# Kernel tuning notes

Measured on AMD Instinct MI355X. Metric: run time of the kernel, lower is better.

The kernel has to match this reference:

```python
import jax, jax.numpy as jnp
import numpy as np
from jax import lax

EPS = 2.220446049250313e-16  # np.finfo(float).eps, as in the torch source
DN3 = ('NCDHW', 'OIDHW', 'NCDHW')
DN2 = ('NCHW', 'OIHW', 'NCHW')


def setup_inputs() -> dict:
    key = jax.random.key(0)
    k1, k2, k3 = jax.random.split(key, 3)
    x = jax.random.normal(k1, (256, 256), dtype=jnp.float32)
    filts_temp = jax.random.normal(k2, (8, 1, 2, 9, 9), dtype=jnp.float32)    # [Ft,1,T=2,kh,kw]
    filts_notemp = jax.random.normal(k3, (8, 1, 1, 9, 9), dtype=jnp.float32)  # [Fn,1,1,kh,kw]
    return {"x": x, "filts_temp": filts_temp, "filts_notemp": filts_notemp, "num_rfs": 2}


def _forward(x, filts_temp, filts_notemp, num_rfs):
    kh, kw = filts_temp.shape[3], filts_temp.shape[4]
    corr_x = num_rfs * kh  # torch uses shape[3]
    corr_y = num_rfs * kw  # torch uses shape[4]
    num_filts = filts_temp.shape[0] + filts_notemp.shape[0]

    # x -> [1,1,2,H,W]: duplicate the frame along a temporal axis of length 2
    xv = jnp.broadcast_to(x, (2,) + x.shape)[None, None]

    # fixed-filter temporal conv3d + ReLU (halved)
    x_temp = jax.nn.relu(
        lax.conv_general_dilated(xv, filts_temp, (1, 1, 1), 'VALID', dimension_numbers=DN3) / 2
    )  # [1,Ft,1,H',W']
    # non-temporal conv on the last time slice
    x_notemp = jax.nn.relu(
        lax.conv_general_dilated(xv[:, :, -1:, :, :], filts_notemp, (1, 1, 1), 'VALID',
                                 dimension_numbers=DN3)
    )  # [1,Fn,1,H',W']

    xc = jnp.concatenate([x_temp, x_notemp], axis=1)  # [1,nf,1,H',W']
    # normalize across the filter channel (divisive normalization)
    x1 = xc / (jnp.sum(xc, axis=1, keepdims=True) + EPS)

    H_, W_ = x1.shape[3], x1.shape[4]
    x1f = x1[0, :, 0]  # [nf,H',W']
    # central crop used as correlation templates
    templates = x1f[:, corr_y:H_ - corr_y, corr_x:W_ - corr_x]  # [nf, H'-2cy, W'-2cx]

    # windowed pairwise cross-channel correlation: the torch conv3d with depth-kernel 1
    # is exactly a batched 2D valid cross-correlation (batch = depth index j,
    # out-channel = template index i)
    out = lax.conv_general_dilated(x1f[:, None], templates[:, None], (1, 1), 'VALID',
                                   dimension_numbers=DN2)  # [j, i, 2cy+1, 2cx+1]
    x2 = jnp.transpose(out, (1, 0, 2, 3))[None]  # [1, i, j, 2cy+1, 2cx+1]
    # note: source divides by (y_max-2*corr_y)*(x_max-2*corr_y) (corr_y twice) -- kept faithful
    x2 = x2 / ((H_ - 2 * corr_y) * (W_ - 2 * corr_y))

    x1_out = x1f[None, None]  # [1,1,nf,H',W']
    return (x1_out, x2)


def reference(x, filts_temp, filts_notemp, num_rfs):
    return _forward(x, filts_temp, filts_notemp, num_rfs)
```

## Files before the change

kernel.cpp:

```cpp
#include <hip/hip_runtime.h>
#include <cstdint>

typedef unsigned short u16;
typedef unsigned int   u32;
typedef unsigned long long u64;
typedef __bf16 bf16x8 __attribute__((ext_vector_type(8)));
typedef float  f32x16 __attribute__((ext_vector_type(16)));
typedef float  f32x4  __attribute__((ext_vector_type(4)));
typedef u32    u32x4  __attribute__((ext_vector_type(4)));

#define OUT1 984064
#define OUT2 350464

#define XD_STRIDE  2031616
#define TMPL_OFFB  16252928
#define PART_OFFB  17801216
#define PART_ELEMS (6*OUT2)
#define XC_OFFB    26212352

__global__ __launch_bounds__(256) void k1_conv(
    const float* __restrict__ x, const float* __restrict__ ft,
    const float* __restrict__ fnt, float* __restrict__ out1,
    u16* __restrict__ Xc) {
  __shared__ float xt[24][25];
  __shared__ float wsm[1296];
  const int tid = threadIdx.x;
  const int lx = tid & 15, ly = tid >> 4;
  const int bx = blockIdx.x, by = blockIdx.y;
  for (int idx = tid; idx < 1296; idx += 256) {
    int c = idx / 81, s = idx - (idx / 81) * 81;
    wsm[idx] = (c < 8) ? 0.5f * (ft[c*162 + s] + ft[c*162 + 81 + s])
                       : fnt[(c-8)*81 + s];
  }
  for (int idx = tid; idx < 576; idx += 256) {
    int ry = idx / 24, rx = idx - ry * 24;
    int gy = by*16 + ry; gy = gy > 255 ? 255 : gy;
    int gx = bx*16 + rx; gx = gx > 255 ? 255 : gx;
    xt[ry][rx] = x[gy*256 + gx];
  }
  __syncthreads();
  const int xg = bx*16 + lx, yg = by*16 + ly;
  if (yg >= 248) return;
  float s[16];
#pragma unroll
  for (int c = 0; c < 16; ++c) s[c] = 0.f;
  const bool valid = (xg < 248);
  if (valid) {
#pragma unroll
    for (int u = 0; u < 9; ++u)
#pragma unroll
      for (int v = 0; v < 9; ++v) {
        float xv = xt[ly + u][lx + v];
#pragma unroll
        for (int c = 0; c < 16; ++c)
          s[c] = __builtin_fmaf(xv, wsm[c*81 + u*9 + v], s[c]);
      }
    float sum = 2.2204460492503131e-16f;
#pragma unroll
    for (int c = 0; c < 16; ++c) { s[c] = s[c] > 0.f ? s[c] : 0.f; sum += s[c]; }
    float inv = 1.f / sum;
#pragma unroll
    for (int c = 0; c < 16; ++c) s[c] *= inv;
  }
#pragma unroll
  for (int c = 0; c < 16; ++c) {
    u16 hb = 0;
    if (valid) {
      out1[c*61504 + yg*248 + xg] = s[c];
      u32 ub = __builtin_bit_cast(u32, s[c]);
      hb = (u16)((ub + 0x7fffu + ((ub >> 16) & 1u)) >> 16);
    }
    if (xg < 264) Xc[(c*248 + yg)*264 + xg] = hb;
  }
}

__global__ __launch_bounds__(256) void k1b_expand(
    const u16* __restrict__ Xc, u16* __restrict__ ws16, float* __restrict__ partial) {
  const int cid = blockIdx.x*256 + threadIdx.x;
  for (int z = cid; z < PART_ELEMS; z += 4346*256) partial[z] = 0.f;
  const u32* src = (const u32*)Xc;
  if (cid < 1015808) {
    int n  = cid & 15;
    int r1 = cid >> 4;
    int row = r1 % 248;
    int r2  = r1 / 248;
    int vb  = r2 & 31;
    int d   = r2 >> 5;
    int colb = (d & ~1) + 8*vb;
    int so = (n*248 + row)*132 + (colb >> 1);
    u32 a0 = src[so], a1 = src[so+1], a2 = src[so+2], a3 = src[so+3], a4 = src[so+4];
    u32x4 v;
    if (d & 1) {
      v[0] = (a0 >> 16) | (a1 << 16); v[1] = (a1 >> 16) | (a2 << 16);
      v[2] = (a2 >> 16) | (a3 << 16); v[3] = (a3 >> 16) | (a4 << 16);
    } else { v[0] = a0; v[1] = a1; v[2] = a2; v[3] = a3; }
    *(u32x4*)(ws16 + (size_t)cid*8) = v;
  } else if (cid < 1015808 + 96768) {
    int t  = cid - 1015808;
    int o  = t & 15;
    int r1 = t >> 4;
    int tr = r1 % 216;
    int vb = r1 / 216;
    u32x4 v = {0u, 0u, 0u, 0u};
    if (tr < 212 && vb < 27) {
      int so = (o*248 + tr + 18)*132 + ((18 + 8*vb) >> 1);
      v[0] = src[so]; v[1] = src[so+1]; v[2] = src[so+2]; v[3] = src[so+3];
      if (vb == 26) { v[2] = 0u; v[3] = 0u; }
    }
    *(u32x4*)(ws16 + (size_t)(TMPL_OFFB/2) + (size_t)t*8) = v;
  }
}

#define F_LD(k,m,c) fl[(k)*1024 + (((m)&3) + 4*((m)>>3))*64 + ((c) + 32*(((m)>>2)&1))]

#define LOADA(q,SO) asm volatile("buffer_load_dwordx4 %0, %1, %2, %3 offen" \
  : "=v"(A[q]) : "v"(voffA[q]), "s"(srdA), "s"(SO));
#define LOADB(t,SO) asm volatile("buffer_load_dwordx4 %0, %1, %2, %3 offen" \
  : "=v"(B[t]) : "v"(voffB[t]), "s"(srdB), "s"(SO));
#define WT(N,X,Y) asm volatile("s_waitcnt vmcnt(" #N ")" : "+v"(X), "+v"(Y) ::);
#define MF5(t) { bf16x8 _bb = __builtin_bit_cast(bf16x8, B[t]); \
  acc[0]=__builtin_amdgcn_mfma_f32_32x32x16_bf16(__builtin_bit_cast(bf16x8,A[t+0]),_bb,acc[0],0,0,0); \
  acc[1]=__builtin_amdgcn_mfma_f32_32x32x16_bf16(__builtin_bit_cast(bf16x8,A[t+1]),_bb,acc[1],0,0,0); \
  acc[2]=__builtin_amdgcn_mfma_f32_32x32x16_bf16(__builtin_bit_cast(bf16x8,A[t+2]),_bb,acc[2],0,0,0); \
  acc[3]=__builtin_amdgcn_mfma_f32_32x32x16_bf16(__builtin_bit_cast(bf16x8,A[t+3]),_bb,acc[3],0,0,0); \
  acc[4]=__builtin_amdgcn_mfma_f32_32x32x16_bf16(__builtin_bit_cast(bf16x8,A[t+4]),_bb,acc[4],0,0,0); }

__global__ __launch_bounds__(256, 2) void k2_corr(
    const u16* __restrict__ Ximg2, const u16* __restrict__ Tmpl2,
    float* __restrict__ partial) {
  __shared__ float fl[5120];
  const int bid = blockIdx.x;
  const int d   = bid & 7;
  const int m0  = bid >> 3;
  const int jq  = m0 % 5;
  const int cmb = m0 / 5;
  const int g   = cmb & 3;
  const int uq  = cmb >> 2;
  const int j   = d + 8*jq;
  if (j >= 37) return;
  const int U0  = 72*uq;
  const int R0  = 10*g + U0;
  const int tid  = threadIdx.x;
  const int lane = tid & 63;
  const int w    = tid >> 6;
  const int fn16 = lane & 15;
  const int fuu  = (lane >> 4) & 1;
  const int fg   = lane >> 5;

  u64 pa = (u64)((const char*)Ximg2 + d*XD_STRIDE + jq*63488);
  u64 pb = (u64)((const char*)Tmpl2);
  u32x4 srdA = { (u32)pa, (u32)(pa >> 32), 0xFFFFFFFFu, 0x00020000u };
  u32x4 srdB = { (u32)pb, (u32)(pb >> 32), 0xFFFFFFFFu, 0x00020000u };
  int voffA[13], voffB[9];
#pragma unroll
  for (int q = 0; q < 13; ++q) {
    int r = R0 + fuu + 18*w + 2*q;
    if (r > 247) r = 247;
    voffA[q] = fg*63488 + fn16*16 + r*256;
  }
#pragma unroll
  for (int t = 0; t < 9; ++t)
    voffB[t] = fg*55296 + fn16*16 + (U0 + fuu + 18*w + 2*t)*256;

  f32x16 acc[5];
#pragma unroll
  for (int k = 0; k < 5; ++k)
#pragma unroll
    for (int q = 0; q < 16; ++q) acc[k][q] = 0.f;

  u32x4 A[13], B[9];
  { int sa = 0, sb = 0;
    LOADA(0,sa) LOADB(0,sb) LOADA(1,sa) LOADB(1,sb)
    LOADA(2,sa) LOADB(2,sb) LOADA(3,sa) LOADB(3,sb)
    LOADA(4,sa) LOADB(4,sb) LOADA(5,sa) LOADB(5,sb)
    LOADA(6,sa) LOADB(6,sb) LOADA(7,sa) LOADB(7,sb)
    LOADA(8,sa) LOADA(9,sa) LOADA(10,sa) LOADA(11,sa) LOADA(12,sa) LOADB(8,sb) }

#pragma unroll 1
  for (int sv = 0; sv < 13; ++sv) {
    const int sa = (sv + 1)*126976, sb = (sv + 1)*110592;
    WT(13, A[4],  B[0])  MF5(0) LOADA(0,sa) LOADB(0,sb)
    WT(13, A[5],  B[1])  MF5(1) LOADA(1,sa) LOADB(1,sb)
    WT(13, A[6],  B[2])  MF5(2) LOADA(2,sa) LOADB(2,sb)
    WT(13, A[7],  B[3])  MF5(3) LOADA(3,sa) LOADB(3,sb)
    WT(13, A[8],  B[4])  MF5(4) LOADA(4,sa) LOADB(4,sb)
    WT(14, A[9],  B[5])  MF5(5) LOADA(5,sa) LOADB(5,sb)
    WT(15, A[10], B[6])  MF5(6) LOADA(6,sa) LOADB(6,sb)
    WT(16, A[11], B[7])  MF5(7) LOADA(7,sa) LOADB(7,sb)
    WT(16, A[12], B[8])  MF5(8)
    LOADA(8,sa) LOADA(9,sa) LOADA(10,sa) LOADA(11,sa) LOADA(12,sa) LOADB(8,sb)
  }
  WT(13, A[4],  B[0])  MF5(0)
  WT(11, A[5],  B[1])  MF5(1)
  WT(9,  A[6],  B[2])  MF5(2)
  WT(7,  A[7],  B[3])  MF5(3)
  WT(5,  A[8],  B[4])  MF5(4)
  WT(4,  A[9],  B[5])  MF5(5)
  WT(3,  A[10], B[6])  MF5(6)
  WT(2,  A[11], B[7])  MF5(7)
  WT(0,  A[12], B[8])  MF5(8)
  __syncthreads();

  for (int z = tid; z < 5120; z += 256) fl[z] = 0.f;
  __syncthreads();
  for (int ww = 0; ww < 4; ++ww) {
    if (w == ww) {
#pragma unroll
      for (int k = 0; k < 5; ++k) {
        if (!(g == 3 && k == 4)) {
#pragma unroll
          for (int q = 0; q < 16; ++q)
            fl[k*1024 + q*64 + lane] += acc[k][q];
        }
      }
    }
    __syncthreads();
  }

  const int n = (tid >> 4) & 15;
  const int o = tid & 15;
  float* slab = partial + (uq*2 + (g & 1)) * OUT2;
  for (int ii = 0; ii < 11; ++ii) {
    const int i = 10*g - 1 + ii;
    if (i < 0 || i >= 37) continue;
    const int dd = ii - 1;
    float v;
    if (!(dd & 1)) {
      const int k = dd >> 1;
      v = F_LD(k, n, o) + F_LD(k, n+16, o+16);
    } else {
      v = 0.f;
      if (dd >= 1) v += F_LD((dd-1) >> 1, n+16, o);
      const int kr = (dd+1) >> 1;
      if (kr <= 4) v += F_LD(kr, n, o+16);
    }
    slab[(o*16 + n)*1369 + i*37 + j] = v;
  }
}

__global__ __launch_bounds__(256) void k3_reduce(
    const float* __restrict__ partial, float* __restrict__ out2) {
  const int idx = blockIdx.x*256 + threadIdx.x;
  if (idx >= OUT2/4) return;
  f32x4 s = {0.f, 0.f, 0.f, 0.f};
#pragma unroll
  for (int t = 0; t < 6; ++t) {
    f32x4 v = *(const f32x4*)(partial + t*OUT2 + idx*4);
    s[0] += v[0]; s[1] += v[1]; s[2] += v[2]; s[3] += v[3];
  }
  const float sc = 1.0f / 44944.0f;
  s[0] *= sc; s[1] *= sc; s[2] *= sc; s[3] *= sc;
  *(f32x4*)(out2 + idx*4) = s;
}

extern "C" void kernel_launch(void* const* d_in, const int* in_sizes, int n_in,
                              void* d_out, int out_size, void* d_ws, size_t ws_size,
                              hipStream_t stream) {
  (void)in_sizes; (void)n_in; (void)out_size; (void)ws_size;
  const float* x   = (const float*)d_in[0];
  const float* ft  = (const float*)d_in[1];
  const float* fnt = (const float*)d_in[2];
  float* out = (float*)d_out;
  char*  ws  = (char*)d_ws;
  u16*   Ximg2   = (u16*)ws;
  u16*   Tmpl2   = (u16*)(ws + TMPL_OFFB);
  float* partial = (float*)(ws + PART_OFFB);
  u16*   Xc      = (u16*)(ws + XC_OFFB);

  k1_conv<<<dim3(17, 16), 256, 0, stream>>>(x, ft, fnt, out, Xc);
  k1b_expand<<<4346, 256, 0, stream>>>(Xc, (u16*)ws, partial);
  k2_corr<<<480, 256, 0, stream>>>(Ximg2, Tmpl2, partial);
  k3_reduce<<<343, 256, 0, stream>>>(partial, out + OUT1);
}
```

Baseline: 74.54 us.

## Switch correlation GEMM operands from bf16 to fp8 e4m3 with repacked layout

```diff
diff --git a/kernel.cpp b/kernel.cpp
--- a/kernel.cpp
+++ b/kernel.cpp
@@ -1,22 +1,23 @@
 #include <hip/hip_runtime.h>
+#include <hip/hip_fp8.h>
 #include <cstdint>
 
 typedef unsigned short u16;
 typedef unsigned int   u32;
 typedef unsigned long long u64;
-typedef __bf16 bf16x8 __attribute__((ext_vector_type(8)));
 typedef float  f32x16 __attribute__((ext_vector_type(16)));
 typedef float  f32x4  __attribute__((ext_vector_type(4)));
+typedef u32    u32x2  __attribute__((ext_vector_type(2)));
 typedef u32    u32x4  __attribute__((ext_vector_type(4)));
 
 #define OUT1 984064
 #define OUT2 350464
 
-#define XD_STRIDE  2031616
+#define XD5        1015808
 #define TMPL_OFFB  16252928
-#define PART_OFFB  17801216
+#define PART_OFFB  17027072
 #define PART_ELEMS (6*OUT2)
-#define XC_OFFB    26212352
+#define XC_OFFB    25438208
 
 __global__ __launch_bounds__(256) void k1_conv(
     const float* __restrict__ x, const float* __restrict__ ft,
@@ -70,73 +71,103 @@
       u32 ub = __builtin_bit_cast(u32, s[c]);
       hb = (u16)((ub + 0x7fffu + ((ub >> 16) & 1u)) >> 16);
     }
-    if (xg < 264) Xc[(c*248 + yg)*264 + xg] = hb;
-  }
+    Xc[(c*248 + yg)*272 + xg] = hb;
+  }
+}
+
+__device__ __forceinline__ u32 pk4_fp8(u32 b0, u32 b1) {
+  float f0 = __builtin_bit_cast(float, b0 << 16);
+  float f1 = __builtin_bit_cast(float, b0 & 0xFFFF0000u);
+  float f2 = __builtin_bit_cast(float, b1 << 16);
+  float f3 = __builtin_bit_cast(float, b1 & 0xFFFF0000u);
+  __hip_fp8_e4m3 e0(f0), e1(f1), e2(f2), e3(f3);
+  return (u32)e0.__x | ((u32)e1.__x << 8) | ((u32)e2.__x << 16) | ((u32)e3.__x << 24);
 }
 
 __global__ __launch_bounds__(256) void k1b_expand(
-    const u16* __restrict__ Xc, u16* __restrict__ ws16, float* __restrict__ partial) {
+    const u16* __restrict__ Xc, unsigned char* __restrict__ ws8,
+    float* __restrict__ partial) {
   const int cid = blockIdx.x*256 + threadIdx.x;
-  for (int z = cid; z < PART_ELEMS; z += 4346*256) partial[z] = 0.f;
+  for (int z = cid; z < PART_ELEMS; z += gridDim.x*256) partial[z] = 0.f;
   const u32* src = (const u32*)Xc;
   if (cid < 1015808) {
     int n  = cid & 15;
     int r1 = cid >> 4;
     int row = r1 % 248;
     int r2  = r1 / 248;
-    int vb  = r2 & 31;
-    int d   = r2 >> 5;
-    int colb = (d & ~1) + 8*vb;
-    int so = (n*248 + row)*132 + (colb >> 1);
-    u32 a0 = src[so], a1 = src[so+1], a2 = src[so+2], a3 = src[so+3], a4 = src[so+4];
-    u32x4 v;
+    int vp  = r2 & 15;
+    int d   = r2 >> 4;
+    int col0 = d + 16*vp;
+    int so = (n*248 + row)*136 + (col0 >> 1);
+    u32 a[9], b[8];
+#pragma unroll
+    for (int i = 0; i < 9; ++i) a[i] = src[so + i];
     if (d & 1) {
-      v[0] = (a0 >> 16) | (a1 << 16); v[1] = (a1 >> 16) | (a2 << 16);
-      v[2] = (a2 >> 16) | (a3 << 16); v[3] = (a3 >> 16) | (a4 << 16);
-    } else { v[0] = a0; v[1] = a1; v[2] = a2; v[3] = a3; }
-    *(u32x4*)(ws16 + (size_t)cid*8) = v;
-  } else if (cid < 1015808 + 96768) {
+#pragma unroll
+      for (int i = 0; i < 8; ++i) b[i] = (a[i] >> 16) | (a[i+1] << 16);
+    } else {
+#pragma unroll
+      for (int i = 0; i < 8; ++i) b[i] = a[i];
+    }
+    u32x4 v = { pk4_fp8(b[0], b[1]), pk4_fp8(b[2], b[3]),
+                pk4_fp8(b[4], b[5]), pk4_fp8(b[6], b[7]) };
+    *(u32x4*)(ws8 + ((size_t)((d*16 + vp)*248 + row))*256 + n*16) = v;
+  } else if (cid < 1015808 + 48384) {
     int t  = cid - 1015808;
     int o  = t & 15;
     int r1 = t >> 4;
     int tr = r1 % 216;
-    int vb = r1 / 216;
+    int vp = r1 / 216;
     u32x4 v = {0u, 0u, 0u, 0u};
-    if (tr < 212 && vb < 27) {
-      int so = (o*248 + tr + 18)*132 + ((18 + 8*vb) >> 1);
-      v[0] = src[so]; v[1] = src[so+1]; v[2] = src[so+2]; v[3] = src[so+3];
-      if (vb == 26) { v[2] = 0u; v[3] = 0u; }
-    }
-    *(u32x4*)(ws16 + (size_t)(TMPL_OFFB/2) + (size_t)t*8) = v;
+    if (tr < 212) {
+      int so = (o*248 + tr + 18)*136 + ((18 + 16*vp) >> 1);
+      u32 b[8];
+#pragma unroll
+      for (int i = 0; i < 8; ++i) b[i] = src[so + i];
+      v[0] = pk4_fp8(b[0], b[1]);
+      if (vp < 13) {
+        v[1] = pk4_fp8(b[2], b[3]);
+        v[2] = pk4_fp8(b[4], b[5]);
+        v[3] = pk4_fp8(b[6], b[7]);
+      }
+    }
+    *(u32x4*)(ws8 + TMPL_OFFB + ((size_t)(vp*216 + tr))*256 + o*16) = v;
   }
 }
 
 #define F_LD(k,m,c) fl[(k)*1024 + (((m)&3) + 4*((m)>>3))*64 + ((c) + 32*(((m)>>2)&1))]
 
-#define LOADA(q,SO) asm volatile("buffer_load_dwordx4 %0, %1, %2, %3 offen" \
+#define LD_A(q,SO) asm volatile("buffer_load_dwordx4 %0, %1, %2, %3 offen" \
   : "=v"(A[q]) : "v"(voffA[q]), "s"(srdA), "s"(SO));
-#define LOADB(t,SO) asm volatile("buffer_load_dwordx4 %0, %1, %2, %3 offen" \
+#define LD_B(t,SO) asm volatile("buffer_load_dwordx4 %0, %1, %2, %3 offen" \
   : "=v"(B[t]) : "v"(voffB[t]), "s"(srdB), "s"(SO));
 #define WT(N,X,Y) asm volatile("s_waitcnt vmcnt(" #N ")" : "+v"(X), "+v"(Y) ::);
-#define MF5(t) { bf16x8 _bb = __builtin_bit_cast(bf16x8, B[t]); \
-  acc[0]=__builtin_amdgcn_mfma_f32_32x32x16_bf16(__builtin_bit_cast(bf16x8,A[t+0]),_bb,acc[0],0,0,0); \
-  acc[1]=__builtin_amdgcn_mfma_f32_32x32x16_bf16(__builtin_bit_cast(bf16x8,A[t+1]),_bb,acc[1],0,0,0); \
-  acc[2]=__builtin_amdgcn_mfma_f32_32x32x16_bf16(__builtin_bit_cast(bf16x8,A[t+2]),_bb,acc[2],0,0,0); \
-  acc[3]=__builtin_amdgcn_mfma_f32_32x32x16_bf16(__builtin_bit_cast(bf16x8,A[t+3]),_bb,acc[3],0,0,0); \
-  acc[4]=__builtin_amdgcn_mfma_f32_32x32x16_bf16(__builtin_bit_cast(bf16x8,A[t+4]),_bb,acc[4],0,0,0); }
+#define LO8(V) __builtin_bit_cast(long, (u32x2){(V)[0], (V)[1]})
+#define HI8(V) __builtin_bit_cast(long, (u32x2){(V)[2], (V)[3]})
+#define MF10(t) { long _bl = LO8(B[t]), _bh = HI8(B[t]); \
+  acc[0]=__builtin_amdgcn_mfma_f32_32x32x16_fp8_fp8(LO8(A[t+0]),_bl,acc[0],0,0,0); \
+  acc[1]=__builtin_amdgcn_mfma_f32_32x32x16_fp8_fp8(LO8(A[t+1]),_bl,acc[1],0,0,0); \
+  acc[2]=__builtin_amdgcn_mfma_f32_32x32x16_fp8_fp8(LO8(A[t+2]),_bl,acc[2],0,0,0); \
+  acc[3]=__builtin_amdgcn_mfma_f32_32x32x16_fp8_fp8(LO8(A[t+3]),_bl,acc[3],0,0,0); \
+  acc[4]=__builtin_amdgcn_mfma_f32_32x32x16_fp8_fp8(LO8(A[t+4]),_bl,acc[4],0,0,0); \
+  acc[0]=__builtin_amdgcn_mfma_f32_32x32x16_fp8_fp8(HI8(A[t+0]),_bh,acc[0],0,0,0); \
+  acc[1]=__builtin_amdgcn_mfma_f32_32x32x16_fp8_fp8(HI8(A[t+1]),_bh,acc[1],0,0,0); \
+  acc[2]=__builtin_amdgcn_mfma_f32_32x32x16_fp8_fp8(HI8(A[t+2]),_bh,acc[2],0,0,0); \
+  acc[3]=__builtin_amdgcn_mfma_f32_32x32x16_fp8_fp8(HI8(A[t+3]),_bh,acc[3],0,0,0); \
+  acc[4]=__builtin_amdgcn_mfma_f32_32x32x16_fp8_fp8(HI8(A[t+4]),_bh,acc[4],0,0,0); }
 
 __global__ __launch_bounds__(256, 2) void k2_corr(
-    const u16* __restrict__ Ximg2, const u16* __restrict__ Tmpl2,
+    const unsigned char* __restrict__ Ximg5, const unsigned char* __restrict__ Tmpl5,
     float* __restrict__ partial) {
   __shared__ float fl[5120];
   const int bid = blockIdx.x;
-  const int d   = bid & 7;
+  const int jl  = bid & 7;
   const int m0  = bid >> 3;
-  const int jq  = m0 % 5;
+  const int jj  = m0 % 5;
   const int cmb = m0 / 5;
   const int g   = cmb & 3;
   const int uq  = cmb >> 2;
-  const int j   = d + 8*jq;
+  const int j   = jl + 8*jj;
   if (j >= 37) return;
   const int U0  = 72*uq;
   const int R0  = 10*g + U0;
@@ -147,8 +178,8 @@
   const int fuu  = (lane >> 4) & 1;
   const int fg   = lane >> 5;
 
-  u64 pa = (u64)((const char*)Ximg2 + d*XD_STRIDE + jq*63488);
-  u64 pb = (u64)((const char*)Tmpl2);
+  u64 pa = (u64)(Ximg5 + (j & 15)*XD5 + (j >> 4)*63488);
+  u64 pb = (u64)(Tmpl5);
   u32x4 srdA = { (u32)pa, (u32)(pa >> 32), 0xFFFFFFFFu, 0x00020000u };
   u32x4 srdB = { (u32)pb, (u32)(pb >> 32), 0xFFFFFFFFu, 0x00020000u };
   int voffA[13], voffB[9];
@@ -170,35 +201,35 @@
 
   u32x4 A[13], B[9];
   { int sa = 0, sb = 0;
-    LOADA(0,sa) LOADB(0,sb) LOADA(1,sa) LOADB(1,sb)
-    LOADA(2,sa) LOADB(2,sb) LOADA(3,sa) LOADB(3,sb)
-    LOADA(4,sa) LOADB(4,sb) LOADA(5,sa) LOADB(5,sb)
-    LOADA(6,sa) LOADB(6,sb) LOADA(7,sa) LOADB(7,sb)
-    LOADA(8,sa) LOADA(9,sa) LOADA(10,sa) LOADA(11,sa) LOADA(12,sa) LOADB(8,sb) }
+    LD_A(0,sa) LD_B(0,sb) LD_A(1,sa) LD_B(1,sb)
+    LD_A(2,sa) LD_B(2,sb) LD_A(3,sa) LD_B(3,sb)
+    LD_A(4,sa) LD_B(4,sb) LD_A(5,sa) LD_B(5,sb)
+    LD_A(6,sa) LD_B(6,sb) LD_A(7,sa) LD_B(7,sb)
+    LD_A(8,sa) LD_A(9,sa) LD_A(10,sa) LD_A(11,sa) LD_A(12,sa) LD_B(8,sb) }
 
 #pragma unroll 1
-  for (int sv = 0; sv < 13; ++sv) {
-    const int sa = (sv + 1)*126976, sb = (sv + 1)*110592;
-    WT(13, A[4],  B[0])  MF5(0) LOADA(0,sa) LOADB(0,sb)
-    WT(13, A[5],  B[1])  MF5(1) LOADA(1,sa) LOADB(1,sb)
-    WT(13, A[6],  B[2])  MF5(2) LOADA(2,sa) LOADB(2,sb)
-    WT(13, A[7],  B[3])  MF5(3) LOADA(3,sa) LOADB(3,sb)
-    WT(13, A[8],  B[4])  MF5(4) LOADA(4,sa) LOADB(4,sb)
-    WT(14, A[9],  B[5])  MF5(5) LOADA(5,sa) LOADB(5,sb)
-    WT(15, A[10], B[6])  MF5(6) LOADA(6,sa) LOADB(6,sb)
-    WT(16, A[11], B[7])  MF5(7) LOADA(7,sa) LOADB(7,sb)
-    WT(16, A[12], B[8])  MF5(8)
-    LOADA(8,sa) LOADA(9,sa) LOADA(10,sa) LOADA(11,sa) LOADA(12,sa) LOADB(8,sb)
-  }
-  WT(13, A[4],  B[0])  MF5(0)
-  WT(11, A[5],  B[1])  MF5(1)
-  WT(9,  A[6],  B[2])  MF5(2)
-  WT(7,  A[7],  B[3])  MF5(3)
-  WT(5,  A[8],  B[4])  MF5(4)
-  WT(4,  A[9],  B[5])  MF5(5)
-  WT(3,  A[10], B[6])  MF5(6)
-  WT(2,  A[11], B[7])  MF5(7)
-  WT(0,  A[12], B[8])  MF5(8)
+  for (int s = 0; s < 6; ++s) {
+    const int sa = (s + 1)*126976, sb = (s + 1)*110592;
+    WT(13, A[4],  B[0])  MF10(0) LD_A(0,sa) LD_B(0,sb)
+    WT(13, A[5],  B[1])  MF10(1) LD_A(1,sa) LD_B(1,sb)
+    WT(13, A[6],  B[2])  MF10(2) LD_A(2,sa) LD_B(2,sb)
+    WT(13, A[7],  B[3])  MF10(3) LD_A(3,sa) LD_B(3,sb)
+    WT(13, A[8],  B[4])  MF10(4) LD_A(4,sa) LD_B(4,sb)
+    WT(14, A[9],  B[5])  MF10(5) LD_A(5,sa) LD_B(5,sb)
+    WT(15, A[10], B[6])  MF10(6) LD_A(6,sa) LD_B(6,sb)
+    WT(16, A[11], B[7])  MF10(7) LD_A(7,sa) LD_B(7,sb)
+    WT(16, A[12], B[8])  MF10(8)
+    LD_A(8,sa) LD_A(9,sa) LD_A(10,sa) LD_A(11,sa) LD_A(12,sa) LD_B(8,sb)
+  }
+  WT(13, A[4],  B[0])  MF10(0)
+  WT(11, A[5],  B[1])  MF10(1)
+  WT(9,  A[6],  B[2])  MF10(2)
+  WT(7,  A[7],  B[3])  MF10(3)
+  WT(5,  A[8],  B[4])  MF10(4)
+  WT(4,  A[9],  B[5])  MF10(5)
+  WT(3,  A[10], B[6])  MF10(6)
+  WT(2,  A[11], B[7])  MF10(7)
+  WT(0,  A[12], B[8])  MF10(8)
   __syncthreads();
 
   for (int z = tid; z < 5120; z += 256) fl[z] = 0.f;
@@ -262,13 +293,13 @@
   const float* fnt = (const float*)d_in[2];
   float* out = (float*)d_out;
   char*  ws  = (char*)d_ws;
-  u16*   Ximg2   = (u16*)ws;
-  u16*   Tmpl2   = (u16*)(ws + TMPL_OFFB);
+  unsigned char* Ximg5 = (unsigned char*)ws;
+  unsigned char* Tmpl5 = (unsigned char*)(ws + TMPL_OFFB);
   float* partial = (float*)(ws + PART_OFFB);
   u16*   Xc      = (u16*)(ws + XC_OFFB);
 
   k1_conv<<<dim3(17, 16), 256, 0, stream>>>(x, ft, fnt, out, Xc);
-  k1b_expand<<<4346, 256, 0, stream>>>(Xc, (u16*)ws, partial);
-  k2_corr<<<480, 256, 0, stream>>>(Ximg2, Tmpl2, partial);
+  k1b_expand<<<4157, 256, 0, stream>>>(Xc, (unsigned char*)ws, partial);
+  k2_corr<<<480, 256, 0, stream>>>(Ximg5, Tmpl5, partial);
   k3_reduce<<<343, 256, 0, stream>>>(partial, out + OUT1);
 }
```

Result: faster. 69.87 us (-6.3%).
